# Kernel optimization log

Hardware: AMD Instinct MI355X
Metric: run time of the kernel (lower is better)

## Reference

```python
import jax, jax.numpy as jnp
import numpy as np

B, N, ND = 4096, 28, 3        # batch, nodes (2 hands x 14 joints), xyz
ED, DD = 512, 256             # encoder dim, decoder dim
H, DH = 8, 64                 # heads, dim_head (inner = 512)
EDEPTH, DDEPTH = 2, 1
EMLP, DMLP = 4 * ED, 4 * DD
NM = 14                       # num_masked = int(0.5 * 28)


def _ln(x, s, b):
    m = jnp.mean(x, -1, keepdims=True)
    v = jnp.var(x, -1, keepdims=True)
    return (x - m) * jax.lax.rsqrt(v + 1e-5) * s + b


def _transformer(x, a, ln1_s, ln1_b, Wqkv, Wo, bo, ln2_s, ln2_b, W1, b1, W2, b2):
    # pre-norm transformer; adjacency a [b,n,n] enters as an additive attention bias
    b, n, _ = x.shape
    scale = DH ** -0.5
    for i in range(ln1_s.shape[0]):
        h = _ln(x, ln1_s[i], ln1_b[i])
        q, k, v = jnp.split(h @ Wqkv[i], 3, axis=-1)
        q = q.reshape(b, n, H, DH).transpose(0, 2, 1, 3)
        k = k.reshape(b, n, H, DH).transpose(0, 2, 1, 3)
        v = v.reshape(b, n, H, DH).transpose(0, 2, 1, 3)
        dots = jnp.einsum('bhid,bhjd->bhij', q, k) * scale + a[:, None]
        attn = jax.nn.softmax(dots, axis=-1)
        o = jnp.einsum('bhij,bhjd->bhid', attn, v).transpose(0, 2, 1, 3).reshape(b, n, H * DH)
        x = x + o @ Wo[i] + bo[i]
        h2 = _ln(x, ln2_s[i], ln2_b[i])
        x = x + jax.nn.gelu(h2 @ W1[i] + b1[i]) @ W2[i] + b2[i]
    return x


def setup_inputs() -> dict:
    key = jax.random.key(0)
    ks = iter(jax.random.split(key, 40))
    nrm = lambda shp, s=0.02: jax.random.normal(next(ks), shp, dtype=jnp.float32) * s
    x = jax.random.normal(next(ks), (B, N, ND), dtype=jnp.float32)
    a = jax.random.uniform(next(ks), (B, N, N), dtype=jnp.float32)
    perm = jnp.argsort(jax.random.uniform(next(ks), (B, N)), axis=-1).astype(jnp.int32)
    masked_indices, unmasked_indices = perm[:, :NM], perm[:, NM:]
    inp = dict(x=x, a=a, masked_indices=masked_indices, unmasked_indices=unmasked_indices)
    inp.update(
        W_emb=nrm((ND, ED)), b_emb=jnp.zeros((ED,), jnp.float32), pos_emb=nrm((N, ED), 0.02),
        e_ln1_s=jnp.ones((EDEPTH, ED)), e_ln1_b=jnp.zeros((EDEPTH, ED)),
        e_Wqkv=nrm((EDEPTH, ED, 3 * H * DH)), e_Wo=nrm((EDEPTH, H * DH, ED)), e_bo=jnp.zeros((EDEPTH, ED)),
        e_ln2_s=jnp.ones((EDEPTH, ED)), e_ln2_b=jnp.zeros((EDEPTH, ED)),
        e_W1=nrm((EDEPTH, ED, EMLP)), e_b1=jnp.zeros((EDEPTH, EMLP)),
        e_W2=nrm((EDEPTH, EMLP, ED)), e_b2=jnp.zeros((EDEPTH, ED)),
        enc2dec_W=nrm((ED, DD)), enc2dec_b=jnp.zeros((DD,), jnp.float32),
        mask_token=nrm((DD,), 1.0), dec_pos_emb=nrm((N, DD), 0.02),
        d_ln1_s=jnp.ones((DDEPTH, DD)), d_ln1_b=jnp.zeros((DDEPTH, DD)),
        d_Wqkv=nrm((DDEPTH, DD, 3 * H * DH)), d_Wo=nrm((DDEPTH, H * DH, DD)), d_bo=jnp.zeros((DDEPTH, DD)),
        d_ln2_s=jnp.ones((DDEPTH, DD)), d_ln2_b=jnp.zeros((DDEPTH, DD)),
        d_W1=nrm((DDEPTH, DD, DMLP)), d_b1=jnp.zeros((DDEPTH, DMLP)),
        d_W2=nrm((DDEPTH, DMLP, DD)), d_b2=jnp.zeros((DDEPTH, DD)),
        pred_W=nrm((DD, ND)), pred_b=jnp.zeros((ND,), jnp.float32),
    )
    return inp


def reference(x, a, masked_indices, unmasked_indices,
              W_emb, b_emb, pos_emb,
              e_ln1_s, e_ln1_b, e_Wqkv, e_Wo, e_bo, e_ln2_s, e_ln2_b, e_W1, e_b1, e_W2, e_b2,
              enc2dec_W, enc2dec_b, mask_token, dec_pos_emb,
              d_ln1_s, d_ln1_b, d_Wqkv, d_Wo, d_bo, d_ln2_s, d_ln2_b, d_W1, d_b1, d_W2, d_b2,
              pred_W, pred_b):
    # node embedding (1x1 conv over nodes == per-node linear) + positional embedding
    tokens = x @ W_emb + b_emb + pos_emb                                   # [B,N,ED]
    unm_tok = jnp.take_along_axis(tokens, unmasked_indices[:, :, None], axis=1)  # [B,N-NM,ED]
    masked_nodes = jnp.take_along_axis(x, masked_indices[:, :, None], axis=1)    # [B,NM,ND]
    # batched adjacency slicing (replaces the per-sample python loop in torch)
    unmasked_a = jax.vmap(lambda ai, ii: ai[ii[:, None], ii[None, :]])(a, unmasked_indices)
    enc = _transformer(unm_tok, unmasked_a,
                       e_ln1_s, e_ln1_b, e_Wqkv, e_Wo, e_bo, e_ln2_s, e_ln2_b, e_W1, e_b1, e_W2, e_b2)
    dec_tok = enc @ enc2dec_W + enc2dec_b                                  # [B,N-NM,DD]
    mask_toks = mask_token + dec_pos_emb[masked_indices]                   # [B,NM,DD]
    # NOTE: faithful to original: unmasked pos-emb tokens are computed but NOT used in the cat
    decoder_tokens = jnp.concatenate([mask_toks, dec_tok], axis=1)         # [B,N,DD]
    decoded = _transformer(decoder_tokens, a,
                           d_ln1_s, d_ln1_b, d_Wqkv, d_Wo, d_bo, d_ln2_s, d_ln2_b, d_W1, d_b1, d_W2, d_b2)
    mt = jnp.take_along_axis(decoded, masked_indices[:, :, None], axis=1)  # [B,NM,DD]
    masked_pred = mt @ pred_W + pred_b                                     # [B,NM,ND]
    recon_loss = jnp.mean((masked_pred - masked_nodes) ** 2)
    return (decoder_tokens, masked_nodes, masked_indices, masked_pred, recon_loss)
```

## Files before the change

kernel.cpp:

```cpp
#include <hip/hip_runtime.h>
#include <math.h>

#define B_TOT 4096
#define N_SEQ 28
#define NDIM 3
#define ED 512
#define DD 256
#define NH 8
#define DHD 64
#define EMLP 2048
#define DMLP 1024
#define NM 14
#define NU 14

typedef __attribute__((ext_vector_type(8))) short short8;
typedef __attribute__((ext_vector_type(4))) float f32x4;
typedef unsigned short ushort_t;
typedef unsigned int uint_t;

__device__ __forceinline__ float gelu_f(float x) {
    float t = 0.7978845608028654f * (x + 0.044715f * x * x * x);
    float e = __expf(2.0f * t);
    float th = 1.0f - 2.0f / (e + 1.0f);
    return 0.5f * x * (1.0f + th);
}
__device__ __forceinline__ ushort_t f2bf(float f) {
    union { float f; uint_t u; } c; c.f = f;
    uint_t u = c.u;
    return (ushort_t)((u + 0x7FFFu + ((u >> 16) & 1u)) >> 16);
}
__device__ __forceinline__ float bf2f(ushort_t h) {
    union { uint_t u; float f; } c; c.u = ((uint_t)h) << 16;
    return c.f;
}
__device__ __forceinline__ float bf_lo(uint_t u) {
    union { uint_t u; float f; } c; c.u = u << 16;
    return c.f;
}
__device__ __forceinline__ float bf_hi(uint_t u) {
    union { uint_t u; float f; } c; c.u = u & 0xFFFF0000u;
    return c.f;
}
__device__ __forceinline__ void gl_lds16(const ushort_t* g, ushort_t* l) {
    __builtin_amdgcn_global_load_lds(
        (const __attribute__((address_space(1))) unsigned int*)g,
        (__attribute__((address_space(3))) unsigned int*)l, 16, 0, 0);
}

__global__ void k_zero(float* p) { p[threadIdx.x] = 0.0f; }
__global__ void k_final(const float* acc, float* out) {
    out[0] = acc[0] * (1.0f / (float)(B_TOT * NM * NDIM));
}

__global__ void k_wconv(const float* __restrict__ W, ushort_t* __restrict__ Wt, int K, int N) {
    __shared__ float tile[32][33];
    int n0 = blockIdx.x * 32, k0 = blockIdx.y * 32;
    int tr = threadIdx.x >> 5, tc = threadIdx.x & 31;
#pragma unroll
    for (int i = 0; i < 4; ++i)
        tile[tr + i * 8][tc] = W[(size_t)(k0 + tr + i * 8) * N + n0 + tc];
    __syncthreads();
#pragma unroll
    for (int i = 0; i < 4; ++i)
        Wt[(size_t)(n0 + tr + i * 8) * K + k0 + tc] = f2bf(tile[tc][tr + i * 8]);
}

__global__ void k_embed(const float* __restrict__ x, const float* __restrict__ a,
                        const int* __restrict__ mi, const int* __restrict__ ui,
                        const float* __restrict__ W_emb, const float* __restrict__ b_emb,
                        const float* __restrict__ pos_emb,
                        ushort_t* __restrict__ X, float* __restrict__ ua,
                        float* __restrict__ out_mn, float* __restrict__ out_midx,
                        int base) {
    int s = blockIdx.x;
    int g = base + s;
    int t = threadIdx.x;
    for (int i = 0; i < NU; ++i) {
        int u = ui[g * NU + i];
        float x0 = x[((size_t)g * N_SEQ + u) * NDIM + 0];
        float x1 = x[((size_t)g * N_SEQ + u) * NDIM + 1];
        float x2 = x[((size_t)g * N_SEQ + u) * NDIM + 2];
        for (int d = t; d < ED; d += 256) {
            X[((size_t)s * NU + i) * ED + d] = f2bf(
                x0 * W_emb[d] + x1 * W_emb[ED + d] + x2 * W_emb[2 * ED + d]
                + b_emb[d] + pos_emb[(size_t)u * ED + d]);
        }
    }
    for (int idx = t; idx < NU * NU; idx += 256) {
        int i = idx / NU, j = idx % NU;
        int uii = ui[g * NU + i], ujj = ui[g * NU + j];
        ua[(size_t)s * NU * NU + idx] = a[(size_t)g * N_SEQ * N_SEQ + (size_t)uii * N_SEQ + ujj];
    }
    for (int idx = t; idx < NM * NDIM; idx += 256) {
        int i = idx / NDIM, c = idx % NDIM;
        int m = mi[g * NM + i];
        out_mn[((size_t)g * NM + i) * NDIM + c] = x[((size_t)g * N_SEQ + m) * NDIM + c];
    }
    for (int i = t; i < NM; i += 256) {
        out_midx[(size_t)g * NM + i] = (float)mi[g * NM + i];
    }
}

template <int D>
__global__ void k_ln(const ushort_t* __restrict__ in, ushort_t* __restrict__ out,
                     const float* __restrict__ sc, const float* __restrict__ bi, int M) {
    int wave = threadIdx.x >> 6;
    int lane = threadIdx.x & 63;
    int row = blockIdx.x * 4 + wave;
    if (row >= M) return;
    constexpr int PL = D / 64;
    const ushort_t* rp = in + (size_t)row * D + lane * PL;
    uint_t u[PL / 2];
    if (PL == 8) *(uint4*)u = *(const uint4*)rp;
    else *(uint2*)u = *(const uint2*)rp;
    float v[PL];
    float sum = 0.f, sq = 0.f;
#pragma unroll
    for (int q = 0; q < PL / 2; ++q) {
        v[2 * q] = bf_lo(u[q]);
        v[2 * q + 1] = bf_hi(u[q]);
    }
#pragma unroll
    for (int j = 0; j < PL; ++j) { sum += v[j]; sq += v[j] * v[j]; }
#pragma unroll
    for (int o = 32; o >= 1; o >>= 1) {
        sum += __shfl_xor(sum, o);
        sq += __shfl_xor(sq, o);
    }
    float mean = sum * (1.0f / D);
    float var = sq * (1.0f / D) - mean * mean;
    float r = rsqrtf(var + 1e-5f);
    uint_t w[PL / 2];
#pragma unroll
    for (int q = 0; q < PL / 2; ++q) {
        int d = lane * PL + 2 * q;
        float a0 = (v[2 * q] - mean) * r * sc[d] + bi[d];
        float a1 = (v[2 * q + 1] - mean) * r * sc[d + 1] + bi[d + 1];
        w[q] = (uint_t)f2bf(a0) | ((uint_t)f2bf(a1) << 16);
    }
    ushort_t* op = out + (size_t)row * D + lane * PL;
    if (PL == 8) *(uint4*)op = *(uint4*)w;
    else *(uint2*)op = *(uint2*)w;
}

template <int ACT>
__global__ __launch_bounds__(256) void k_gemm_mfma(
    const ushort_t* __restrict__ A, const ushort_t* __restrict__ Wt,
    const float* __restrict__ bias, const ushort_t* __restrict__ res,
    ushort_t* __restrict__ Cout, int M, int N, int K) {
    __shared__ __align__(16) ushort_t smem[24576];

    const int t = threadIdx.x;
    const int gx = gridDim.x;
    int flat = blockIdx.y * gx + blockIdx.x;
    int nwg = gx * gridDim.y;
    int q8 = nwg >> 3, r8 = nwg & 7;
    int xcd = flat & 7, loc = flat >> 3;
    int wg = (xcd < r8 ? xcd * (q8 + 1) : r8 * (q8 + 1) + (xcd - r8) * q8) + loc;
    const int bm = wg / gx, bn = wg % gx;

    const int lane = t & 63;
    const int wave = t >> 6;
    const int wr = wave >> 1, wc = wave & 1;
    const int l15 = lane & 15;
    const int g4 = lane >> 4;
    const int kq = (g4 ^ ((l15 >> 1) & 3)) * 8;

    const int srow = wave * 32 + (lane >> 2);
    const int scol = ((lane & 3) ^ ((lane >> 3) & 3)) * 8;
    const ushort_t* Ag = A + (size_t)(bm * 128 + srow) * K + scol;
    const ushort_t* Bg = Wt + (size_t)(bn * 128 + srow) * K + scol;
    const int wb0 = (wave * 32) * 32;
    const int wb1 = (wave * 32 + 16) * 32;

    f32x4 acc[4][4] = {};
    const int nt = K >> 5;

#define STAGE(tile, idx)                                          \
    do {                                                          \
        int k0_ = (tile) << 5;                                    \
        ushort_t* Ab_ = smem + (idx) * 8192;                      \
        ushort_t* Bb_ = Ab_ + 4096;                               \
        gl_lds16(Ag + k0_, Ab_ + wb0);                            \
        gl_lds16(Ag + (size_t)16 * K + k0_, Ab_ + wb1);           \
        gl_lds16(Bg + k0_, Bb_ + wb0);                            \
        gl_lds16(Bg + (size_t)16 * K + k0_, Bb_ + wb1);           \
    } while (0)

    STAGE(0, 0);
    STAGE(1, 1);

    int cur = 0;
    for (int tt = 0; tt < nt; ++tt) {
        if (tt + 1 < nt) asm volatile("s_waitcnt vmcnt(4)" ::: "memory");
        else             asm volatile("s_waitcnt vmcnt(0)" ::: "memory");
        __builtin_amdgcn_s_barrier();
        __builtin_amdgcn_sched_barrier(0);
        if (tt + 2 < nt) {
            int nidx = cur + 2; if (nidx >= 3) nidx -= 3;
            STAGE(tt + 2, nidx);
        }
        __builtin_amdgcn_sched_barrier(0);
        const ushort_t* Ac = smem + cur * 8192;
        const ushort_t* Bc = Ac + 4096;
        short8 af[4], bfr[4];
#pragma unroll
        for (int m = 0; m < 4; ++m)
            af[m] = *(const short8*)&Ac[(wr * 64 + m * 16 + l15) * 32 + kq];
#pragma unroll
        for (int n = 0; n < 4; ++n)
            bfr[n] = *(const short8*)&Bc[(wc * 64 + n * 16 + l15) * 32 + kq];
#pragma unroll
        for (int m = 0; m < 4; ++m)
#pragma unroll
            for (int n = 0; n < 4; ++n)
                acc[m][n] = __builtin_amdgcn_mfma_f32_16x16x32_bf16(af[m], bfr[n], acc[m][n], 0, 0, 0);
        if (++cur == 3) cur = 0;
    }
#undef STAGE

    __builtin_amdgcn_sched_barrier(0);
    __builtin_amdgcn_s_barrier();

    ushort_t* Cs = smem;
    const int erow0 = wr * 64, ecol0 = wc * 64;
#pragma unroll
    for (int m = 0; m < 4; ++m)
#pragma unroll
        for (int n = 0; n < 4; ++n)
#pragma unroll
            for (int r = 0; r < 4; ++r) {
                float v = acc[m][n][r];
                float o = __shfl_xor(v, 1);
                if (!(l15 & 1)) {
                    uint_t pk = (uint_t)f2bf(v) | ((uint_t)f2bf(o) << 16);
                    *(uint_t*)&Cs[(erow0 + m * 16 + g4 * 4 + r) * 136 + ecol0 + n * 16 + l15] = pk;
                }
            }
    __builtin_amdgcn_s_barrier();

    const int row = t >> 1, half = t & 1;
    const int grow = bm * 128 + row;
    const int gc0 = bn * 128 + half * 64;
    const ushort_t* rres = res ? res + (size_t)grow * N + gc0 : (const ushort_t*)0;
    ushort_t* gout = Cout + (size_t)grow * N + gc0;
#pragma unroll
    for (int c = 0; c < 8; ++c) {
        uint4 pv = *(const uint4*)&Cs[row * 136 + half * 64 + c * 8];
        uint_t* pw = (uint_t*)&pv;
        float vv[8];
#pragma unroll
        for (int q = 0; q < 4; ++q) { vv[2 * q] = bf_lo(pw[q]); vv[2 * q + 1] = bf_hi(pw[q]); }
        if (bias) {
#pragma unroll
            for (int j = 0; j < 8; ++j) vv[j] += bias[gc0 + c * 8 + j];
        }
        if (res) {
            uint4 rv = *(const uint4*)(rres + c * 8);
            uint_t* pr = (uint_t*)&rv;
#pragma unroll
            for (int q = 0; q < 4; ++q) { vv[2 * q] += bf_lo(pr[q]); vv[2 * q + 1] += bf_hi(pr[q]); }
        }
        if (ACT == 1) {
#pragma unroll
            for (int j = 0; j < 8; ++j) vv[j] = gelu_f(vv[j]);
        }
        uint4 ov;
        uint_t* po = (uint_t*)&ov;
#pragma unroll
        for (int q = 0; q < 4; ++q)
            po[q] = (uint_t)f2bf(vv[2 * q]) | ((uint_t)f2bf(vv[2 * q + 1]) << 16);
        *(uint4*)(gout + c * 8) = ov;
    }
}

template <int NT>
__global__ __launch_bounds__(256) void k_attn_mfma(
    const ushort_t* __restrict__ qkv, const float* __restrict__ bias,
    ushort_t* __restrict__ O) {
    constexpr int NTP = (NT + 15) & ~15;
    constexpr int MT = NTP / 16;
    constexpr int QS = 72;
    constexpr int VS = 40;
    __shared__ __align__(16) ushort_t smem[4 * NTP * QS * 2 + 4 * 64 * VS];
    ushort_t* Qs = smem;
    ushort_t* Ks = smem + 4 * NTP * QS;
    ushort_t* Vs = Ks + 4 * NTP * QS;
    ushort_t* Ps = smem;

    const int s = blockIdx.x, hg = blockIdx.y;
    const int t = threadIdx.x;
    const int wave = t >> 6, lane = t & 63;
    const int l15 = lane & 15, g4 = lane >> 4;

    const ushort_t* qb = qkv + (size_t)s * NT * 1536 + hg * 256;
    for (int c = t; c < 64 * NT; c += 256) {
        int c8 = c & 7;
        int rem = c >> 3;
        int r = rem % NT;
        int ph = rem / NT;
        int h = ph & 3, p = ph >> 2;
        uint4 v = *(const uint4*)(qb + (size_t)r * 1536 + p * 512 + h * 64 + c8 * 8);
        ushort_t* dst = (p ? Ks : Qs) + (h * NTP + r) * QS + c8 * 8;
        *(uint4*)dst = v;
    }
    const ushort_t* vrow = qkv + (size_t)s * NT * 1536 + 1024 + hg * 256;
    for (int c = t; c < 4 * 64 * (32 - NT); c += 256) {
        int p = c % (32 - NT);
        int hd = c / (32 - NT);
        Vs[hd * VS + NT + p] = 0;
    }
    for (int c = t; c < 4 * NT * 8; c += 256) {
        int c8 = c & 7;
        int r = (c >> 3) % NT;
        int h = (c >> 3) / NT;
        uint4 v = *(const uint4*)(vrow + (size_t)r * 1536 + h * 64 + c8 * 8);
        const uint_t* pv = (const uint_t*)&v;
#pragma unroll
        for (int j = 0; j < 4; ++j) {
            Vs[(h * 64 + c8 * 8 + 2 * j) * VS + r] = (ushort_t)(pv[j] & 0xFFFFu);
            Vs[(h * 64 + c8 * 8 + 2 * j + 1) * VS + r] = (ushort_t)(pv[j] >> 16);
        }
    }
    __syncthreads();

    const int h = wave;
    const ushort_t* Qh = Qs + h * NTP * QS;
    const ushort_t* Kh = Ks + h * NTP * QS;
    const ushort_t* Vh = Vs + h * 64 * VS;
    ushort_t* Ph = Ps + h * NTP * VS;

    f32x4 sacc[MT][MT] = {};
#pragma unroll
    for (int ks = 0; ks < 2; ++ks) {
        short8 qf[MT], kf[MT];
#pragma unroll
        for (int m = 0; m < MT; ++m)
            qf[m] = *(const short8*)&Qh[(m * 16 + l15) * QS + ks * 32 + g4 * 8];
#pragma unroll
        for (int n = 0; n < MT; ++n)
            kf[n] = *(const short8*)&Kh[(n * 16 + l15) * QS + ks * 32 + g4 * 8];
#pragma unroll
        for (int m = 0; m < MT; ++m)
#pragma unroll
            for (int n = 0; n < MT; ++n)
                sacc[m][n] = __builtin_amdgcn_mfma_f32_16x16x32_bf16(qf[m], kf[n], sacc[m][n], 0, 0, 0);
    }

    const float* bp = bias + (size_t)s * NT * NT;
    float prv[MT][MT][4];
#pragma unroll
    for (int m = 0; m < MT; ++m) {
#pragma unroll
        for (int r = 0; r < 4; ++r) {
            int i = m * 16 + g4 * 4 + r;
            float sv[MT];
#pragma unroll
            for (int n = 0; n < MT; ++n) {
                int j = n * 16 + l15;
                sv[n] = (i < NT && j < NT) ? sacc[m][n][r] * 0.125f + bp[i * NT + j] : -1e30f;
            }
            float mx = sv[0];
            if (MT > 1) mx = fmaxf(mx, sv[MT - 1]);
#pragma unroll
            for (int o = 1; o < 16; o <<= 1) mx = fmaxf(mx, __shfl_xor(mx, o));
            float sum = 0.f;
#pragma unroll
            for (int n = 0; n < MT; ++n) {
                float e = (sv[n] > -1e29f) ? __expf(sv[n] - mx) : 0.f;
                prv[m][n][r] = e;
                sum += e;
            }
#pragma unroll
            for (int o = 1; o < 16; o <<= 1) sum += __shfl_xor(sum, o);
            float rs = sum > 0.f ? 1.0f / sum : 0.f;
#pragma unroll
            for (int n = 0; n < MT; ++n) prv[m][n][r] *= rs;
        }
    }
    __syncthreads();

    if (NTP == 16) {
        for (int z = lane; z < 16 * 8; z += 64) {
            int i = z >> 3, jw = z & 7;
            *(uint_t*)&Ph[i * VS + 16 + jw * 2] = 0;
        }
    }
#pragma unroll
    for (int m = 0; m < MT; ++m)
#pragma unroll
        for (int n = 0; n < MT; ++n)
#pragma unroll
            for (int r = 0; r < 4; ++r)
                Ph[(m * 16 + g4 * 4 + r) * VS + n * 16 + l15] = f2bf(prv[m][n][r]);
    __syncthreads();

    f32x4 oacc[MT][4] = {};
    {
        short8 pf[MT], vf[4];
#pragma unroll
        for (int m = 0; m < MT; ++m)
            pf[m] = *(const short8*)&Ph[(m * 16 + l15) * VS + g4 * 8];
#pragma unroll
        for (int nd = 0; nd < 4; ++nd)
            vf[nd] = *(const short8*)&Vh[(nd * 16 + l15) * VS + g4 * 8];
#pragma unroll
        for (int m = 0; m < MT; ++m)
#pragma unroll
            for (int nd = 0; nd < 4; ++nd)
                oacc[m][nd] = __builtin_amdgcn_mfma_f32_16x16x32_bf16(pf[m], vf[nd], oacc[m][nd], 0, 0, 0);
    }

    ushort_t* Ob = O + (size_t)s * NT * 512 + hg * 256 + h * 64;
#pragma unroll
    for (int m = 0; m < MT; ++m)
#pragma unroll
        for (int r = 0; r < 4; ++r) {
            int i = m * 16 + g4 * 4 + r;
            if (i < NT) {
#pragma unroll
                for (int nd = 0; nd < 4; ++nd)
                    Ob[(size_t)i * 512 + nd * 16 + l15] = f2bf(oacc[m][nd][r]);
            }
        }
}

__global__ void k_build_dec(const ushort_t* __restrict__ dec_tok, const float* __restrict__ mask_token,
                            const float* __restrict__ dec_pos, const int* __restrict__ mi,
                            ushort_t* __restrict__ Xd, float* __restrict__ out0, int base) {
    int s = blockIdx.x;
    int g = base + s;
    int t = threadIdx.x;
    for (int idx = t; idx < N_SEQ * DD; idx += 256) {
        int i = idx / DD, d = idx % DD;
        float v;
        if (i < NM) {
            int m = mi[g * NM + i];
            v = mask_token[d] + dec_pos[(size_t)m * DD + d];
        } else {
            v = bf2f(dec_tok[((size_t)s * NU + (i - NM)) * DD + d]);
        }
        Xd[((size_t)s * N_SEQ + i) * DD + d] = f2bf(v);
        out0[((size_t)g * N_SEQ + i) * DD + d] = v;
    }
}

__global__ void k_pred(const ushort_t* __restrict__ Xd, const int* __restrict__ mi,
                       const float* __restrict__ pW, const float* __restrict__ pb,
                       const float* __restrict__ mn, float* __restrict__ out_pred,
                       float* __restrict__ loss, int base, int Bc) {
    int tid = blockIdx.x * 256 + threadIdx.x;
    int total = Bc * NM * NDIM;
    float part = 0.f;
    if (tid < total) {
        int c = tid % NDIM;
        int r = tid / NDIM;
        int i = r % NM;
        int s = r / NM;
        int g = base + s;
        int m = mi[g * NM + i];
        const ushort_t* row = Xd + ((size_t)s * N_SEQ + m) * DD;
        float acc = pb[c];
        for (int k = 0; k < DD; ++k) acc += bf2f(row[k]) * pW[k * NDIM + c];
        out_pred[((size_t)g * NM + i) * NDIM + c] = acc;
        float d = acc - mn[((size_t)g * NM + i) * NDIM + c];
        part = d * d;
    }
    __shared__ float red[256];
    red[threadIdx.x] = part;
    __syncthreads();
    for (int o = 128; o > 0; o >>= 1) {
        if (threadIdx.x < o) red[threadIdx.x] += red[threadIdx.x + o];
        __syncthreads();
    }
    if (threadIdx.x == 0) atomicAdd(loss, red[0]);
}

extern "C" void kernel_launch(void* const* d_in, const int* in_sizes, int n_in,
                              void* d_out, int out_size, void* d_ws, size_t ws_size,
                              hipStream_t stream) {
    const float* x       = (const float*)d_in[0];
    const float* a       = (const float*)d_in[1];
    const int*   mi      = (const int*)d_in[2];
    const int*   ui      = (const int*)d_in[3];
    const float* W_emb   = (const float*)d_in[4];
    const float* b_emb   = (const float*)d_in[5];
    const float* pos_emb = (const float*)d_in[6];
    const float* e_ln1_s = (const float*)d_in[7];
    const float* e_ln1_b = (const float*)d_in[8];
    const float* e_Wqkv  = (const float*)d_in[9];
    const float* e_Wo    = (const float*)d_in[10];
    const float* e_bo    = (const float*)d_in[11];
    const float* e_ln2_s = (const float*)d_in[12];
    const float* e_ln2_b = (const float*)d_in[13];
    const float* e_W1    = (const float*)d_in[14];
    const float* e_b1    = (const float*)d_in[15];
    const float* e_W2    = (const float*)d_in[16];
    const float* e_b2    = (const float*)d_in[17];
    const float* e2d_W   = (const float*)d_in[18];
    const float* e2d_b   = (const float*)d_in[19];
    const float* mask_tok= (const float*)d_in[20];
    const float* dec_pos = (const float*)d_in[21];
    const float* d_ln1_s = (const float*)d_in[22];
    const float* d_ln1_b = (const float*)d_in[23];
    const float* d_Wqkv  = (const float*)d_in[24];
    const float* d_Wo    = (const float*)d_in[25];
    const float* d_bo    = (const float*)d_in[26];
    const float* d_ln2_s = (const float*)d_in[27];
    const float* d_ln2_b = (const float*)d_in[28];
    const float* d_W1    = (const float*)d_in[29];
    const float* d_b1    = (const float*)d_in[30];
    const float* d_W2    = (const float*)d_in[31];
    const float* d_b2    = (const float*)d_in[32];
    const float* pred_W  = (const float*)d_in[33];
    const float* pred_b  = (const float*)d_in[34];

    float* out0 = (float*)d_out;
    float* out1 = out0 + (size_t)B_TOT * N_SEQ * DD;
    float* out2 = out1 + (size_t)B_TOT * NM * NDIM;
    float* out3 = out2 + (size_t)B_TOT * NM;
    float* out4 = out3 + (size_t)B_TOT * NM * NDIM;

    char* wp = (char*)d_ws;
    size_t off = 0;
    auto alloc = [&](size_t bytes) {
        size_t o = off;
        off = (off + bytes + 255) & ~(size_t)255;
        return (void*)(wp + o);
    };
    float* loss_acc = (float*)alloc(64 * 4);
    ushort_t* wt_eqkv = (ushort_t*)alloc((size_t)2 * 1536 * 512 * 2);
    ushort_t* wt_ewo  = (ushort_t*)alloc((size_t)2 * 512 * 512 * 2);
    ushort_t* wt_ew1  = (ushort_t*)alloc((size_t)2 * 2048 * 512 * 2);
    ushort_t* wt_ew2  = (ushort_t*)alloc((size_t)2 * 512 * 2048 * 2);
    ushort_t* wt_dqkv = (ushort_t*)alloc((size_t)1536 * 256 * 2);
    ushort_t* wt_dwo  = (ushort_t*)alloc((size_t)256 * 512 * 2);
    ushort_t* wt_dw1  = (ushort_t*)alloc((size_t)1024 * 256 * 2);
    ushort_t* wt_dw2  = (ushort_t*)alloc((size_t)256 * 1024 * 2);
    ushort_t* wt_e2d  = (ushort_t*)alloc((size_t)256 * 512 * 2);
    size_t fixed_bytes = off;

    const size_t per_seq = 2 * (7168 + 3584 + 7168 + 43008 + 14336) + 4 * 196;
    int Bc = B_TOT;
    while (Bc > 64 && fixed_bytes + (size_t)Bc * per_seq + 8192 > ws_size) Bc >>= 1;

    ushort_t* Xbuf   = (ushort_t*)alloc((size_t)Bc * 7168 * 2);
    ushort_t* Dbuf   = (ushort_t*)alloc((size_t)Bc * 3584 * 2);
    float*    uabuf  = (float*)alloc((size_t)Bc * 196 * 4);
    ushort_t* Hbuf   = (ushort_t*)alloc((size_t)Bc * 7168 * 2);
    ushort_t* QKVbuf = (ushort_t*)alloc((size_t)Bc * 43008 * 2);
    ushort_t* Obuf   = (ushort_t*)alloc((size_t)Bc * 14336 * 2);

    k_zero<<<1, 64, 0, stream>>>(loss_acc);

    for (int l = 0; l < 2; ++l) {
        k_wconv<<<dim3(1536 / 32, 512 / 32), 256, 0, stream>>>(e_Wqkv + (size_t)l * 512 * 1536, wt_eqkv + (size_t)l * 1536 * 512, 512, 1536);
        k_wconv<<<dim3(512 / 32, 512 / 32), 256, 0, stream>>>(e_Wo + (size_t)l * 512 * 512, wt_ewo + (size_t)l * 512 * 512, 512, 512);
        k_wconv<<<dim3(2048 / 32, 512 / 32), 256, 0, stream>>>(e_W1 + (size_t)l * 512 * 2048, wt_ew1 + (size_t)l * 2048 * 512, 512, 2048);
        k_wconv<<<dim3(512 / 32, 2048 / 32), 256, 0, stream>>>(e_W2 + (size_t)l * 2048 * 512, wt_ew2 + (size_t)l * 512 * 2048, 2048, 512);
    }
    k_wconv<<<dim3(1536 / 32, 256 / 32), 256, 0, stream>>>(d_Wqkv, wt_dqkv, 256, 1536);
    k_wconv<<<dim3(256 / 32, 512 / 32), 256, 0, stream>>>(d_Wo, wt_dwo, 512, 256);
    k_wconv<<<dim3(1024 / 32, 256 / 32), 256, 0, stream>>>(d_W1, wt_dw1, 256, 1024);
    k_wconv<<<dim3(256 / 32, 1024 / 32), 256, 0, stream>>>(d_W2, wt_dw2, 1024, 256);
    k_wconv<<<dim3(256 / 32, 512 / 32), 256, 0, stream>>>(e2d_W, wt_e2d, 512, 256);

    const int nchunk = B_TOT / Bc;
    for (int c = 0; c < nchunk; ++c) {
        int base = c * Bc;
        int M = Bc * NU;
        int Md = Bc * N_SEQ;

        k_embed<<<Bc, 256, 0, stream>>>(x, a, mi, ui, W_emb, b_emb, pos_emb,
                                        Xbuf, uabuf, out1, out2, base);
        for (int l = 0; l < 2; ++l) {
            k_ln<ED><<<M / 4, 256, 0, stream>>>(Xbuf, Hbuf, e_ln1_s + l * ED, e_ln1_b + l * ED, M);
            k_gemm_mfma<0><<<dim3(1536 / 128, M / 128), 256, 0, stream>>>(
                Hbuf, wt_eqkv + (size_t)l * 1536 * 512, nullptr, nullptr, QKVbuf, M, 1536, ED);
            k_attn_mfma<NU><<<dim3(Bc, 2), 256, 0, stream>>>(QKVbuf, uabuf, Obuf);
            k_gemm_mfma<0><<<dim3(ED / 128, M / 128), 256, 0, stream>>>(
                Obuf, wt_ewo + (size_t)l * 512 * 512, e_bo + l * ED, Xbuf, Xbuf, M, ED, 512);
            k_ln<ED><<<M / 4, 256, 0, stream>>>(Xbuf, Hbuf, e_ln2_s + l * ED, e_ln2_b + l * ED, M);
            k_gemm_mfma<1><<<dim3(EMLP / 128, M / 128), 256, 0, stream>>>(
                Hbuf, wt_ew1 + (size_t)l * 2048 * 512, e_b1 + l * EMLP, nullptr, QKVbuf, M, EMLP, ED);
            k_gemm_mfma<0><<<dim3(ED / 128, M / 128), 256, 0, stream>>>(
                QKVbuf, wt_ew2 + (size_t)l * 512 * 2048, e_b2 + l * ED, Xbuf, Xbuf, M, ED, EMLP);
        }
        k_gemm_mfma<0><<<dim3(DD / 128, M / 128), 256, 0, stream>>>(
            Xbuf, wt_e2d, e2d_b, nullptr, Dbuf, M, DD, ED);
        k_build_dec<<<Bc, 256, 0, stream>>>(Dbuf, mask_tok, dec_pos, mi, Xbuf, out0, base);
        k_ln<DD><<<Md / 4, 256, 0, stream>>>(Xbuf, Hbuf, d_ln1_s, d_ln1_b, Md);
        k_gemm_mfma<0><<<dim3(1536 / 128, Md / 128), 256, 0, stream>>>(
            Hbuf, wt_dqkv, nullptr, nullptr, QKVbuf, Md, 1536, DD);
        k_attn_mfma<N_SEQ><<<dim3(Bc, 2), 256, 0, stream>>>(QKVbuf, a + (size_t)base * N_SEQ * N_SEQ, Obuf);
        k_gemm_mfma<0><<<dim3(DD / 128, Md / 128), 256, 0, stream>>>(
            Obuf, wt_dwo, d_bo, Xbuf, Xbuf, Md, DD, 512);
        k_ln<DD><<<Md / 4, 256, 0, stream>>>(Xbuf, Hbuf, d_ln2_s, d_ln2_b, Md);
        k_gemm_mfma<1><<<dim3(DMLP / 128, Md / 128), 256, 0, stream>>>(
            Hbuf, wt_dw1, d_b1, nullptr, QKVbuf, Md, DMLP, DD);
        k_gemm_mfma<0><<<dim3(DD / 128, Md / 128), 256, 0, stream>>>(
            QKVbuf, wt_dw2, d_b2, Xbuf, Xbuf, Md, DD, DMLP);
        int tot = Bc * NM * NDIM;
        k_pred<<<(tot + 255) / 256, 256, 0, stream>>>(
            Xbuf, mi, pred_W, pred_b, out1, out3, loss_acc, base, Bc);
    }
    k_final<<<1, 1, 0, stream>>>(loss_acc, out4);
}
```

Measured before the change: 2.731 ms.

## Enlarge GEMM tile to 256x128 with per-wave 64x128 outputs and packed bf16 convert

The MFMA GEMM moves from a 128x128 block tile split 2x2 across waves to a 256x128 tile, where each wave owns 64 rows across all 128 columns. The B fragments in LDS are now shared by all four waves, which raises MFMA work per LDS byte loaded. The epilogue writes the output in two 128-row halves through the same LDS staging area and uses the hardware v_cvt_pk_bf16_f32 instruction for float-to-bf16 packing. The costs are twice as many accumulator registers, which can lower occupancy, half as many workgroups, and a minimum chunk size raised to 128 so M stays a multiple of 256.

```diff
diff --git a/kernel.cpp b/kernel.cpp
--- a/kernel.cpp
+++ b/kernel.cpp
@@ -40,6 +40,11 @@
 __device__ __forceinline__ float bf_hi(uint_t u) {
     union { uint_t u; float f; } c; c.u = u & 0xFFFF0000u;
     return c.f;
+}
+__device__ __forceinline__ uint_t cvtpk(float lo, float hi) {
+    uint_t r;
+    asm volatile("v_cvt_pk_bf16_f32 %0, %1, %2" : "=v"(r) : "v"(lo), "v"(hi));
+    return r;
 }
 __device__ __forceinline__ void gl_lds16(const ushort_t* g, ushort_t* l) {
     __builtin_amdgcn_global_load_lds(
@@ -148,7 +153,7 @@
     const ushort_t* __restrict__ A, const ushort_t* __restrict__ Wt,
     const float* __restrict__ bias, const ushort_t* __restrict__ res,
     ushort_t* __restrict__ Cout, int M, int N, int K) {
-    __shared__ __align__(16) ushort_t smem[24576];
+    __shared__ __align__(16) ushort_t smem[36864];
 
     const int t = threadIdx.x;
     const int gx = gridDim.x;
@@ -161,30 +166,30 @@
 
     const int lane = t & 63;
     const int wave = t >> 6;
-    const int wr = wave >> 1, wc = wave & 1;
     const int l15 = lane & 15;
     const int g4 = lane >> 4;
     const int kq = (g4 ^ ((l15 >> 1) & 3)) * 8;
 
-    const int srow = wave * 32 + (lane >> 2);
     const int scol = ((lane & 3) ^ ((lane >> 3) & 3)) * 8;
-    const ushort_t* Ag = A + (size_t)(bm * 128 + srow) * K + scol;
-    const ushort_t* Bg = Wt + (size_t)(bn * 128 + srow) * K + scol;
-    const int wb0 = (wave * 32) * 32;
-    const int wb1 = (wave * 32 + 16) * 32;
-
-    f32x4 acc[4][4] = {};
+    const ushort_t* Ag = A + (size_t)(bm * 256 + wave * 64 + (lane >> 2)) * K + scol;
+    const ushort_t* Bg = Wt + (size_t)(bn * 128 + wave * 32 + (lane >> 2)) * K + scol;
+    const int wbA = (wave * 64) * 32;
+    const int wbB = (wave * 32) * 32;
+
+    f32x4 acc[4][8] = {};
     const int nt = K >> 5;
 
-#define STAGE(tile, idx)                                          \
-    do {                                                          \
-        int k0_ = (tile) << 5;                                    \
-        ushort_t* Ab_ = smem + (idx) * 8192;                      \
-        ushort_t* Bb_ = Ab_ + 4096;                               \
-        gl_lds16(Ag + k0_, Ab_ + wb0);                            \
-        gl_lds16(Ag + (size_t)16 * K + k0_, Ab_ + wb1);           \
-        gl_lds16(Bg + k0_, Bb_ + wb0);                            \
-        gl_lds16(Bg + (size_t)16 * K + k0_, Bb_ + wb1);           \
+#define STAGE(tile, idx)                                              \
+    do {                                                              \
+        int k0_ = (tile) << 5;                                        \
+        ushort_t* Ab_ = smem + (idx) * 12288;                         \
+        ushort_t* Bb_ = Ab_ + 8192;                                   \
+        gl_lds16(Ag + k0_, Ab_ + wbA);                                \
+        gl_lds16(Ag + (size_t)16 * K + k0_, Ab_ + wbA + 512);         \
+        gl_lds16(Ag + (size_t)32 * K + k0_, Ab_ + wbA + 1024);        \
+        gl_lds16(Ag + (size_t)48 * K + k0_, Ab_ + wbA + 1536);        \
+        gl_lds16(Bg + k0_, Bb_ + wbB);                                \
+        gl_lds16(Bg + (size_t)16 * K + k0_, Bb_ + wbB + 512);         \
     } while (0)
 
     STAGE(0, 0);
@@ -192,7 +197,7 @@
 
     int cur = 0;
     for (int tt = 0; tt < nt; ++tt) {
-        if (tt + 1 < nt) asm volatile("s_waitcnt vmcnt(4)" ::: "memory");
+        if (tt + 1 < nt) asm volatile("s_waitcnt vmcnt(6)" ::: "memory");
         else             asm volatile("s_waitcnt vmcnt(0)" ::: "memory");
         __builtin_amdgcn_s_barrier();
         __builtin_amdgcn_sched_barrier(0);
@@ -200,20 +205,19 @@
             int nidx = cur + 2; if (nidx >= 3) nidx -= 3;
             STAGE(tt + 2, nidx);
         }
-        __builtin_amdgcn_sched_barrier(0);
-        const ushort_t* Ac = smem + cur * 8192;
-        const ushort_t* Bc = Ac + 4096;
-        short8 af[4], bfr[4];
+        const ushort_t* Ac = smem + cur * 12288;
+        const ushort_t* Bc = Ac + 8192;
+        short8 af[4], bfr[8];
 #pragma unroll
         for (int m = 0; m < 4; ++m)
-            af[m] = *(const short8*)&Ac[(wr * 64 + m * 16 + l15) * 32 + kq];
-#pragma unroll
-        for (int n = 0; n < 4; ++n)
-            bfr[n] = *(const short8*)&Bc[(wc * 64 + n * 16 + l15) * 32 + kq];
+            af[m] = *(const short8*)&Ac[(wave * 64 + m * 16 + l15) * 32 + kq];
+#pragma unroll
+        for (int n = 0; n < 8; ++n)
+            bfr[n] = *(const short8*)&Bc[(n * 16 + l15) * 32 + kq];
 #pragma unroll
         for (int m = 0; m < 4; ++m)
 #pragma unroll
-            for (int n = 0; n < 4; ++n)
+            for (int n = 0; n < 8; ++n)
                 acc[m][n] = __builtin_amdgcn_mfma_f32_16x16x32_bf16(af[m], bfr[n], acc[m][n], 0, 0, 0);
         if (++cur == 3) cur = 0;
     }
@@ -223,54 +227,59 @@
     __builtin_amdgcn_s_barrier();
 
     ushort_t* Cs = smem;
-    const int erow0 = wr * 64, ecol0 = wc * 64;
-#pragma unroll
-    for (int m = 0; m < 4; ++m)
-#pragma unroll
-        for (int n = 0; n < 4; ++n)
-#pragma unroll
-            for (int r = 0; r < 4; ++r) {
-                float v = acc[m][n][r];
-                float o = __shfl_xor(v, 1);
-                if (!(l15 & 1)) {
-                    uint_t pk = (uint_t)f2bf(v) | ((uint_t)f2bf(o) << 16);
-                    *(uint_t*)&Cs[(erow0 + m * 16 + g4 * 4 + r) * 136 + ecol0 + n * 16 + l15] = pk;
-                }
+    const int row = t >> 1, half = t & 1;
+    const int gc0 = bn * 128 + half * 64;
+#pragma unroll
+    for (int hp = 0; hp < 2; ++hp) {
+        if ((wave >> 1) == hp) {
+            const int erow0 = (wave & 1) * 64;
+#pragma unroll
+            for (int m = 0; m < 4; ++m)
+#pragma unroll
+                for (int n = 0; n < 8; ++n)
+#pragma unroll
+                    for (int r = 0; r < 4; ++r) {
+                        float v = acc[m][n][r];
+                        float o = __shfl_xor(v, 1);
+                        if (!(l15 & 1)) {
+                            uint_t pk = cvtpk(v, o);
+                            *(uint_t*)&Cs[(erow0 + m * 16 + g4 * 4 + r) * 136 + n * 16 + l15] = pk;
+                        }
+                    }
+        }
+        __builtin_amdgcn_s_barrier();
+        const int grow = bm * 256 + hp * 128 + row;
+        const ushort_t* rres = res ? res + (size_t)grow * N + gc0 : (const ushort_t*)0;
+        ushort_t* gout = Cout + (size_t)grow * N + gc0;
+#pragma unroll
+        for (int c = 0; c < 8; ++c) {
+            uint4 pv = *(const uint4*)&Cs[row * 136 + half * 64 + c * 8];
+            uint_t* pw = (uint_t*)&pv;
+            float vv[8];
+#pragma unroll
+            for (int q = 0; q < 4; ++q) { vv[2 * q] = bf_lo(pw[q]); vv[2 * q + 1] = bf_hi(pw[q]); }
+            if (bias) {
+#pragma unroll
+                for (int j = 0; j < 8; ++j) vv[j] += bias[gc0 + c * 8 + j];
             }
-    __builtin_amdgcn_s_barrier();
-
-    const int row = t >> 1, half = t & 1;
-    const int grow = bm * 128 + row;
-    const int gc0 = bn * 128 + half * 64;
-    const ushort_t* rres = res ? res + (size_t)grow * N + gc0 : (const ushort_t*)0;
-    ushort_t* gout = Cout + (size_t)grow * N + gc0;
-#pragma unroll
-    for (int c = 0; c < 8; ++c) {
-        uint4 pv = *(const uint4*)&Cs[row * 136 + half * 64 + c * 8];
-        uint_t* pw = (uint_t*)&pv;
-        float vv[8];
-#pragma unroll
-        for (int q = 0; q < 4; ++q) { vv[2 * q] = bf_lo(pw[q]); vv[2 * q + 1] = bf_hi(pw[q]); }
-        if (bias) {
-#pragma unroll
-            for (int j = 0; j < 8; ++j) vv[j] += bias[gc0 + c * 8 + j];
-        }
-        if (res) {
-            uint4 rv = *(const uint4*)(rres + c * 8);
-            uint_t* pr = (uint_t*)&rv;
-#pragma unroll
-            for (int q = 0; q < 4; ++q) { vv[2 * q] += bf_lo(pr[q]); vv[2 * q + 1] += bf_hi(pr[q]); }
-        }
-        if (ACT == 1) {
-#pragma unroll
-            for (int j = 0; j < 8; ++j) vv[j] = gelu_f(vv[j]);
-        }
-        uint4 ov;
-        uint_t* po = (uint_t*)&ov;
-#pragma unroll
-        for (int q = 0; q < 4; ++q)
-            po[q] = (uint_t)f2bf(vv[2 * q]) | ((uint_t)f2bf(vv[2 * q + 1]) << 16);
-        *(uint4*)(gout + c * 8) = ov;
+            if (res) {
+                uint4 rv = *(const uint4*)(rres + c * 8);
+                uint_t* pr = (uint_t*)&rv;
+#pragma unroll
+                for (int q = 0; q < 4; ++q) { vv[2 * q] += bf_lo(pr[q]); vv[2 * q + 1] += bf_hi(pr[q]); }
+            }
+            if (ACT == 1) {
+#pragma unroll
+                for (int j = 0; j < 8; ++j) vv[j] = gelu_f(vv[j]);
+            }
+            uint4 ov;
+            uint_t* po = (uint_t*)&ov;
+#pragma unroll
+            for (int q = 0; q < 4; ++q)
+                po[q] = cvtpk(vv[2 * q], vv[2 * q + 1]);
+            *(uint4*)(gout + c * 8) = ov;
+        }
+        __builtin_amdgcn_s_barrier();
     }
 }
 
@@ -542,7 +551,7 @@
 
     const size_t per_seq = 2 * (7168 + 3584 + 7168 + 43008 + 14336) + 4 * 196;
     int Bc = B_TOT;
-    while (Bc > 64 && fixed_bytes + (size_t)Bc * per_seq + 8192 > ws_size) Bc >>= 1;
+    while (Bc > 128 && fixed_bytes + (size_t)Bc * per_seq + 8192 > ws_size) Bc >>= 1;
 
     ushort_t* Xbuf   = (ushort_t*)alloc((size_t)Bc * 7168 * 2);
     ushort_t* Dbuf   = (ushort_t*)alloc((size_t)Bc * 3584 * 2);
@@ -575,30 +584,30 @@
                                         Xbuf, uabuf, out1, out2, base);
         for (int l = 0; l < 2; ++l) {
             k_ln<ED><<<M / 4, 256, 0, stream>>>(Xbuf, Hbuf, e_ln1_s + l * ED, e_ln1_b + l * ED, M);
-            k_gemm_mfma<0><<<dim3(1536 / 128, M / 128), 256, 0, stream>>>(
+            k_gemm_mfma<0><<<dim3(1536 / 128, M / 256), 256, 0, stream>>>(
                 Hbuf, wt_eqkv + (size_t)l * 1536 * 512, nullptr, nullptr, QKVbuf, M, 1536, ED);
             k_attn_mfma<NU><<<dim3(Bc, 2), 256, 0, stream>>>(QKVbuf, uabuf, Obuf);
-            k_gemm_mfma<0><<<dim3(ED / 128, M / 128), 256, 0, stream>>>(
+            k_gemm_mfma<0><<<dim3(ED / 128, M / 256), 256, 0, stream>>>(
                 Obuf, wt_ewo + (size_t)l * 512 * 512, e_bo + l * ED, Xbuf, Xbuf, M, ED, 512);
             k_ln<ED><<<M / 4, 256, 0, stream>>>(Xbuf, Hbuf, e_ln2_s + l * ED, e_ln2_b + l * ED, M);
-            k_gemm_mfma<1><<<dim3(EMLP / 128, M / 128), 256, 0, stream>>>(
+            k_gemm_mfma<1><<<dim3(EMLP / 128, M / 256), 256, 0, stream>>>(
                 Hbuf, wt_ew1 + (size_t)l * 2048 * 512, e_b1 + l * EMLP, nullptr, QKVbuf, M, EMLP, ED);
-            k_gemm_mfma<0><<<dim3(ED / 128, M / 128), 256, 0, stream>>>(
+            k_gemm_mfma<0><<<dim3(ED / 128, M / 256), 256, 0, stream>>>(
                 QKVbuf, wt_ew2 + (size_t)l * 512 * 2048, e_b2 + l * ED, Xbuf, Xbuf, M, ED, EMLP);
         }
-        k_gemm_mfma<0><<<dim3(DD / 128, M / 128), 256, 0, stream>>>(
+        k_gemm_mfma<0><<<dim3(DD / 128, M / 256), 256, 0, stream>>>(
             Xbuf, wt_e2d, e2d_b, nullptr, Dbuf, M, DD, ED);
         k_build_dec<<<Bc, 256, 0, stream>>>(Dbuf, mask_tok, dec_pos, mi, Xbuf, out0, base);
         k_ln<DD><<<Md / 4, 256, 0, stream>>>(Xbuf, Hbuf, d_ln1_s, d_ln1_b, Md);
-        k_gemm_mfma<0><<<dim3(1536 / 128, Md / 128), 256, 0, stream>>>(
+        k_gemm_mfma<0><<<dim3(1536 / 128, Md / 256), 256, 0, stream>>>(
             Hbuf, wt_dqkv, nullptr, nullptr, QKVbuf, Md, 1536, DD);
         k_attn_mfma<N_SEQ><<<dim3(Bc, 2), 256, 0, stream>>>(QKVbuf, a + (size_t)base * N_SEQ * N_SEQ, Obuf);
-        k_gemm_mfma<0><<<dim3(DD / 128, Md / 128), 256, 0, stream>>>(
+        k_gemm_mfma<0><<<dim3(DD / 128, Md / 256), 256, 0, stream>>>(
             Obuf, wt_dwo, d_bo, Xbuf, Xbuf, Md, DD, 512);
         k_ln<DD><<<Md / 4, 256, 0, stream>>>(Xbuf, Hbuf, d_ln2_s, d_ln2_b, Md);
-        k_gemm_mfma<1><<<dim3(DMLP / 128, Md / 128), 256, 0, stream>>>(
+        k_gemm_mfma<1><<<dim3(DMLP / 128, Md / 256), 256, 0, stream>>>(
             Hbuf, wt_dw1, d_b1, nullptr, QKVbuf, Md, DMLP, DD);
-        k_gemm_mfma<0><<<dim3(DD / 128, Md / 128), 256, 0, stream>>>(
+        k_gemm_mfma<0><<<dim3(DD / 128, Md / 256), 256, 0, stream>>>(
             QKVbuf, wt_dw2, d_b2, Xbuf, Xbuf, Md, DD, DMLP);
         int tot = Bc * NM * NDIM;
         k_pred<<<(tot + 255) / 256, 256, 0, stream>>>(
```

Measured after the change: 4.373 ms. 60.1% more time.

## Write attention output in place into QKV buffer and use hardware bf16 pack

Applied to the files above, without the earlier changes.

The attention kernel now writes its output over the Q slot of the QKV buffer instead of a separate O buffer. The output-projection GEMM reads it through a new lda stride of 1536, which removes the O buffer and shrinks the per-sequence workspace, possibly allowing larger chunks. The GEMM epilogue also replaces the software bf16 rounding with the v_cvt_pk_bf16_f32 instruction, and one sched_barrier in the main loop is removed. In-place writes depend on each attention block finishing its Q reads before overwriting them, and strided A loads may hurt coalescing slightly.

```diff
diff --git a/kernel.cpp b/kernel.cpp
--- a/kernel.cpp
+++ b/kernel.cpp
@@ -40,6 +40,11 @@
 __device__ __forceinline__ float bf_hi(uint_t u) {
     union { uint_t u; float f; } c; c.u = u & 0xFFFF0000u;
     return c.f;
+}
+__device__ __forceinline__ uint_t cvtpk(float lo, float hi) {
+    uint_t r;
+    asm volatile("v_cvt_pk_bf16_f32 %0, %1, %2" : "=v"(r) : "v"(lo), "v"(hi));
+    return r;
 }
 __device__ __forceinline__ void gl_lds16(const ushort_t* g, ushort_t* l) {
     __builtin_amdgcn_global_load_lds(
@@ -147,7 +152,7 @@
 __global__ __launch_bounds__(256) void k_gemm_mfma(
     const ushort_t* __restrict__ A, const ushort_t* __restrict__ Wt,
     const float* __restrict__ bias, const ushort_t* __restrict__ res,
-    ushort_t* __restrict__ Cout, int M, int N, int K) {
+    ushort_t* __restrict__ Cout, int M, int N, int K, int lda) {
     __shared__ __align__(16) ushort_t smem[24576];
 
     const int t = threadIdx.x;
@@ -168,7 +173,7 @@
 
     const int srow = wave * 32 + (lane >> 2);
     const int scol = ((lane & 3) ^ ((lane >> 3) & 3)) * 8;
-    const ushort_t* Ag = A + (size_t)(bm * 128 + srow) * K + scol;
+    const ushort_t* Ag = A + (size_t)(bm * 128 + srow) * lda + scol;
     const ushort_t* Bg = Wt + (size_t)(bn * 128 + srow) * K + scol;
     const int wb0 = (wave * 32) * 32;
     const int wb1 = (wave * 32 + 16) * 32;
@@ -182,7 +187,7 @@
         ushort_t* Ab_ = smem + (idx) * 8192;                      \
         ushort_t* Bb_ = Ab_ + 4096;                               \
         gl_lds16(Ag + k0_, Ab_ + wb0);                            \
-        gl_lds16(Ag + (size_t)16 * K + k0_, Ab_ + wb1);           \
+        gl_lds16(Ag + (size_t)16 * lda + k0_, Ab_ + wb1);         \
         gl_lds16(Bg + k0_, Bb_ + wb0);                            \
         gl_lds16(Bg + (size_t)16 * K + k0_, Bb_ + wb1);           \
     } while (0)
@@ -200,7 +205,6 @@
             int nidx = cur + 2; if (nidx >= 3) nidx -= 3;
             STAGE(tt + 2, nidx);
         }
-        __builtin_amdgcn_sched_barrier(0);
         const ushort_t* Ac = smem + cur * 8192;
         const ushort_t* Bc = Ac + 4096;
         short8 af[4], bfr[4];
@@ -233,7 +237,7 @@
                 float v = acc[m][n][r];
                 float o = __shfl_xor(v, 1);
                 if (!(l15 & 1)) {
-                    uint_t pk = (uint_t)f2bf(v) | ((uint_t)f2bf(o) << 16);
+                    uint_t pk = cvtpk(v, o);
                     *(uint_t*)&Cs[(erow0 + m * 16 + g4 * 4 + r) * 136 + ecol0 + n * 16 + l15] = pk;
                 }
             }
@@ -269,15 +273,14 @@
         uint_t* po = (uint_t*)&ov;
 #pragma unroll
         for (int q = 0; q < 4; ++q)
-            po[q] = (uint_t)f2bf(vv[2 * q]) | ((uint_t)f2bf(vv[2 * q + 1]) << 16);
+            po[q] = cvtpk(vv[2 * q], vv[2 * q + 1]);
         *(uint4*)(gout + c * 8) = ov;
     }
 }
 
 template <int NT>
 __global__ __launch_bounds__(256) void k_attn_mfma(
-    const ushort_t* __restrict__ qkv, const float* __restrict__ bias,
-    ushort_t* __restrict__ O) {
+    ushort_t* __restrict__ qkv, const float* __restrict__ bias) {
     constexpr int NTP = (NT + 15) & ~15;
     constexpr int MT = NTP / 16;
     constexpr int QS = 72;
@@ -411,7 +414,7 @@
                 oacc[m][nd] = __builtin_amdgcn_mfma_f32_16x16x32_bf16(pf[m], vf[nd], oacc[m][nd], 0, 0, 0);
     }
 
-    ushort_t* Ob = O + (size_t)s * NT * 512 + hg * 256 + h * 64;
+    ushort_t* Ob = qkv + (size_t)s * NT * 1536 + hg * 256 + h * 64;
 #pragma unroll
     for (int m = 0; m < MT; ++m)
 #pragma unroll
@@ -420,7 +423,7 @@
             if (i < NT) {
 #pragma unroll
                 for (int nd = 0; nd < 4; ++nd)
-                    Ob[(size_t)i * 512 + nd * 16 + l15] = f2bf(oacc[m][nd][r]);
+                    Ob[(size_t)i * 1536 + nd * 16 + l15] = f2bf(oacc[m][nd][r]);
             }
         }
 }
@@ -540,7 +543,7 @@
     ushort_t* wt_e2d  = (ushort_t*)alloc((size_t)256 * 512 * 2);
     size_t fixed_bytes = off;
 
-    const size_t per_seq = 2 * (7168 + 3584 + 7168 + 43008 + 14336) + 4 * 196;
+    const size_t per_seq = 2 * (7168 + 3584 + 7168 + 43008) + 4 * 196;
     int Bc = B_TOT;
     while (Bc > 64 && fixed_bytes + (size_t)Bc * per_seq + 8192 > ws_size) Bc >>= 1;
 
@@ -549,7 +552,6 @@
     float*    uabuf  = (float*)alloc((size_t)Bc * 196 * 4);
     ushort_t* Hbuf   = (ushort_t*)alloc((size_t)Bc * 7168 * 2);
     ushort_t* QKVbuf = (ushort_t*)alloc((size_t)Bc * 43008 * 2);
-    ushort_t* Obuf   = (ushort_t*)alloc((size_t)Bc * 14336 * 2);
 
     k_zero<<<1, 64, 0, stream>>>(loss_acc);
 
@@ -576,30 +578,30 @@
         for (int l = 0; l < 2; ++l) {
             k_ln<ED><<<M / 4, 256, 0, stream>>>(Xbuf, Hbuf, e_ln1_s + l * ED, e_ln1_b + l * ED, M);
             k_gemm_mfma<0><<<dim3(1536 / 128, M / 128), 256, 0, stream>>>(
-                Hbuf, wt_eqkv + (size_t)l * 1536 * 512, nullptr, nullptr, QKVbuf, M, 1536, ED);
-            k_attn_mfma<NU><<<dim3(Bc, 2), 256, 0, stream>>>(QKVbuf, uabuf, Obuf);
+                Hbuf, wt_eqkv + (size_t)l * 1536 * 512, nullptr, nullptr, QKVbuf, M, 1536, ED, ED);
+            k_attn_mfma<NU><<<dim3(Bc, 2), 256, 0, stream>>>(QKVbuf, uabuf);
             k_gemm_mfma<0><<<dim3(ED / 128, M / 128), 256, 0, stream>>>(
-                Obuf, wt_ewo + (size_t)l * 512 * 512, e_bo + l * ED, Xbuf, Xbuf, M, ED, 512);
+                QKVbuf, wt_ewo + (size_t)l * 512 * 512, e_bo + l * ED, Xbuf, Xbuf, M, ED, 512, 1536);
             k_ln<ED><<<M / 4, 256, 0, stream>>>(Xbuf, Hbuf, e_ln2_s + l * ED, e_ln2_b + l * ED, M);
             k_gemm_mfma<1><<<dim3(EMLP / 128, M / 128), 256, 0, stream>>>(
-                Hbuf, wt_ew1 + (size_t)l * 2048 * 512, e_b1 + l * EMLP, nullptr, QKVbuf, M, EMLP, ED);
+                Hbuf, wt_ew1 + (size_t)l * 2048 * 512, e_b1 + l * EMLP, nullptr, QKVbuf, M, EMLP, ED, ED);
             k_gemm_mfma<0><<<dim3(ED / 128, M / 128), 256, 0, stream>>>(
-                QKVbuf, wt_ew2 + (size_t)l * 512 * 2048, e_b2 + l * ED, Xbuf, Xbuf, M, ED, EMLP);
+                QKVbuf, wt_ew2 + (size_t)l * 512 * 2048, e_b2 + l * ED, Xbuf, Xbuf, M, ED, EMLP, EMLP);
         }
         k_gemm_mfma<0><<<dim3(DD / 128, M / 128), 256, 0, stream>>>(
-            Xbuf, wt_e2d, e2d_b, nullptr, Dbuf, M, DD, ED);
+            Xbuf, wt_e2d, e2d_b, nullptr, Dbuf, M, DD, ED, ED);
         k_build_dec<<<Bc, 256, 0, stream>>>(Dbuf, mask_tok, dec_pos, mi, Xbuf, out0, base);
         k_ln<DD><<<Md / 4, 256, 0, stream>>>(Xbuf, Hbuf, d_ln1_s, d_ln1_b, Md);
         k_gemm_mfma<0><<<dim3(1536 / 128, Md / 128), 256, 0, stream>>>(
-            Hbuf, wt_dqkv, nullptr, nullptr, QKVbuf, Md, 1536, DD);
-        k_attn_mfma<N_SEQ><<<dim3(Bc, 2), 256, 0, stream>>>(QKVbuf, a + (size_t)base * N_SEQ * N_SEQ, Obuf);
+            Hbuf, wt_dqkv, nullptr, nullptr, QKVbuf, Md, 1536, DD, DD);
+        k_attn_mfma<N_SEQ><<<dim3(Bc, 2), 256, 0, stream>>>(QKVbuf, a + (size_t)base * N_SEQ * N_SEQ);
         k_gemm_mfma<0><<<dim3(DD / 128, Md / 128), 256, 0, stream>>>(
-            Obuf, wt_dwo, d_bo, Xbuf, Xbuf, Md, DD, 512);
+            QKVbuf, wt_dwo, d_bo, Xbuf, Xbuf, Md, DD, 512, 1536);
         k_ln<DD><<<Md / 4, 256, 0, stream>>>(Xbuf, Hbuf, d_ln2_s, d_ln2_b, Md);
         k_gemm_mfma<1><<<dim3(DMLP / 128, Md / 128), 256, 0, stream>>>(
-            Hbuf, wt_dw1, d_b1, nullptr, QKVbuf, Md, DMLP, DD);
+            Hbuf, wt_dw1, d_b1, nullptr, QKVbuf, Md, DMLP, DD, DD);
         k_gemm_mfma<0><<<dim3(DD / 128, Md / 128), 256, 0, stream>>>(
-            QKVbuf, wt_dw2, d_b2, Xbuf, Xbuf, Md, DD, DMLP);
+            QKVbuf, wt_dw2, d_b2, Xbuf, Xbuf, Md, DD, DMLP, DMLP);
         int tot = Bc * NM * NDIM;
         k_pred<<<(tot + 255) / 256, 256, 0, stream>>>(
             Xbuf, mi, pred_W, pred_b, out1, out3, loss_acc, base, Bc);
```

New measurement: 2.651 ms. 2.9% less time.
